# Kernel optimization log

Measured on AMD Instinct MI355X. Metric: run time of the kernel, lower is better.

## Reference

```python
import jax, jax.numpy as jnp
import numpy as np

H = 1024        # hidden_dim
MD = 2048       # memory_dim
L = 16384       # memory length == max_length
N = 8           # head_N
# sys.float_info.min underflows to 0.0 in float32, exactly as in the torch
# original (python float * float32 tensor). Kept for faithfulness.
TINY = jnp.float32(2.2250738585072014e-308)


def setup_inputs() -> dict:
    key = jax.random.key(0)
    ks = jax.random.split(key, 12)
    s_h = 1.0 / np.sqrt(H)
    s_m = 1.0 / np.sqrt(MD)
    s_o = 1.0 / np.sqrt(2 * H)
    return {
        "x": jax.random.normal(ks[0], (1, 1, H), jnp.float32),
        "memory": jax.random.normal(ks[1], (L, MD), jnp.float32),
        "Wq": jax.random.uniform(ks[2], (H, H), jnp.float32, -s_h, s_h),
        "bq": jax.random.uniform(ks[3], (H,), jnp.float32, -s_h, s_h),
        "Wk": jax.random.uniform(ks[4], (H, MD), jnp.float32, -s_m, s_m),
        "bk": jax.random.uniform(ks[5], (H,), jnp.float32, -s_m, s_m),
        "Wv": jax.random.uniform(ks[6], (H, MD), jnp.float32, -s_m, s_m),
        "bv": jax.random.uniform(ks[7], (H,), jnp.float32, -s_m, s_m),
        "Wo": jax.random.uniform(ks[8], (H, 2 * H), jnp.float32, -s_o, s_o),
        "bo": jax.random.uniform(ks[9], (H,), jnp.float32, -s_o, s_o),
    }


def reference(x, memory, Wq, bq, Wk, bk, Wv, bv, Wo, bo):
    d = H // N  # per-head dim
    # Q: (1,H) -> (1,d,N) -> (N,1,d), scaled by d**-0.5
    q = x.reshape(1, -1) @ Wq.T + bq
    Q = q.reshape(1, d, N).transpose(2, 0, 1) * (d ** -0.5)
    # K: (L,H) -> (L,d,N) -> (N,d,L)
    K = (memory @ Wk.T + bk).reshape(-1, d, N).transpose(2, 1, 0)
    QK = jnp.einsum('nod,ndl->nol', Q, K)  # (N,1,L)
    # pad mask: 1 where the memory row sums to zero, else 0 (as in torch nonzero-set)
    any_zero = memory.sum(axis=1)
    pad_mask = (any_zero == 0).astype(QK.dtype)[None, None, :]
    QK = QK + pad_mask * TINY
    attn = jax.nn.softmax(QK, axis=-1)
    # V: (L,H) -> (L,d,N) -> (N,L,d)
    V = (memory @ Wv.T + bv).reshape(-1, d, N).transpose(2, 0, 1)
    feat = jnp.einsum('nol,nld->nod', attn, V)      # (N,1,d)
    feat = feat.transpose(1, 2, 0).reshape(1, 1, H)  # (1,1,H)
    ax = jnp.concatenate([x, feat], axis=-1)         # (1,1,2H)
    return jax.nn.relu(ax @ Wo.T + bo)
```

## Files before the change

kernel.cpp:

```cpp
#include <hip/hip_runtime.h>
#include <math.h>

#define LROWS 16384
#define HDIM  1024
#define MDIM  2048
#define RSQRT_D 0.08838834764831844f

#define OFF_W     0
#define OFF_BETA  16384
#define OFF_Z     16392
#define OFF_Q     16400
#define OFF_FEAT  17424
#define OFF_Y     18448
#define OFF_ZP    34832
#define OFF_S2    38928
#define OFF_YBUF  301072

__device__ __forceinline__ float dot4(float4 a, float4 b) {
  return a.x * b.x + a.y * b.y + a.z * b.z + a.w * b.w;
}
__device__ __forceinline__ void fma4(float4& acc, float s, float4 v) {
  acc.x = fmaf(s, v.x, acc.x); acc.y = fmaf(s, v.y, acc.y);
  acc.z = fmaf(s, v.z, acc.z); acc.w = fmaf(s, v.w, acc.w);
}
__device__ __forceinline__ void add4(float4& a, float4 v) {
  a.x += v.x; a.y += v.y; a.z += v.z; a.w += v.w;
}

__global__ __launch_bounds__(256) void kq(const float* __restrict__ x,
                                          const float* __restrict__ Wq,
                                          const float* __restrict__ bq,
                                          float* __restrict__ ws) {
  int tid = threadIdx.x, lane = tid & 63;
  int j = blockIdx.x * 4 + (tid >> 6);
  const float4* xr = (const float4*)x;
  const float4* wr = (const float4*)(Wq + (size_t)j * HDIM);
  float acc = 0.f;
#pragma unroll
  for (int i = 0; i < 4; ++i) {
    int idx = i * 64 + lane;
    acc += dot4(xr[idx], wr[idx]);
  }
#pragma unroll
  for (int off = 32; off; off >>= 1) acc += __shfl_xor(acc, off);
  if (lane == 0) ws[OFF_Q + j] = acc + bq[j];
  if (tid < 64) ws[OFF_W + blockIdx.x * 64 + tid] = 0.f;
}

__global__ __launch_bounds__(256) void kw(const float* __restrict__ Wk,
                                          const float* __restrict__ bk,
                                          float* __restrict__ ws) {
  __shared__ float lds[32];
  int tid = threadIdx.x;
  const float* q = ws + OFF_Q;
  if (blockIdx.x == 256) {
    float b = 0.f;
#pragma unroll
    for (int i = 0; i < 4; ++i) {
      int c = tid + 256 * i;
      b = fmaf(q[c], bk[c], b);
    }
    b += __shfl_xor(b, 8); b += __shfl_xor(b, 16); b += __shfl_xor(b, 32);
    if ((tid & 63) < 8) lds[(tid >> 6) * 8 + (tid & 7)] = b;
    __syncthreads();
    if (tid < 8)
      ws[OFF_BETA + tid] = lds[tid] + lds[8 + tid] + lds[16 + tid] + lds[24 + tid];
    return;
  }
  int mc = blockIdx.x & 7, cc = blockIdx.x >> 3;
  int m = mc * 256 + tid;
  float acc[8];
#pragma unroll
  for (int n = 0; n < 8; ++n) acc[n] = 0.f;
  int c0 = cc * 32;
#pragma unroll
  for (int cb = 0; cb < 32; cb += 8) {
#pragma unroll
    for (int u = 0; u < 8; ++u)
      acc[u] = fmaf(q[c0 + cb + u], Wk[(size_t)(c0 + cb + u) * MDIM + m], acc[u]);
  }
#pragma unroll
  for (int n = 0; n < 8; ++n) atomicAdd(&ws[OFF_W + n * MDIM + m], acc[n]);
}

__global__ __launch_bounds__(256, 4) void kA3(const float* __restrict__ mem,
                                              float* __restrict__ ws) {
  __shared__ float4 wlds[2048];
  int tid = threadIdx.x, lane = tid & 63, wv = tid >> 6;
  int ch = blockIdx.x & 1, rg = blockIdx.x >> 1;
  const float4* wsrc = (const float4*)(ws + OFF_W + ch * 1024);
#pragma unroll
  for (int k = 0; k < 8; ++k) {
    int qi = k * 256 + tid;
    wlds[qi] = wsrc[(qi >> 8) * 512 + (qi & 255)];
  }
  __syncthreads();

  int r0 = rg * 32 + wv * 8;
  const float* base = mem + (size_t)r0 * MDIM + ch * 1024;
  float* sbase = ws + OFF_S2 + (size_t)ch * 131072 + (size_t)r0 * 8;

  float4 mv[4], mvn[4];
#pragma unroll
  for (int i = 0; i < 4; ++i)
    mv[i] = *(const float4*)(base + (i * 64 + lane) * 4);

#pragma unroll
  for (int rl = 0; rl < 8; ++rl) {
    if (rl < 7) {
#pragma unroll
      for (int i = 0; i < 4; ++i)
        mvn[i] = *(const float4*)(base + (size_t)(rl + 1) * MDIM + (i * 64 + lane) * 4);
    }
    float acc[8];
#pragma unroll
    for (int n = 0; n < 8; ++n) acc[n] = 0.f;
#pragma unroll
    for (int pass = 0; pass < 4; ++pass) {
      int cq = pass * 64 + lane;
#pragma unroll
      for (int n = 0; n < 8; ++n) {
        float4 w4 = wlds[n * 256 + cq];
        acc[n] = fmaf(mv[pass].x, w4.x, acc[n]);
        acc[n] = fmaf(mv[pass].y, w4.y, acc[n]);
        acc[n] = fmaf(mv[pass].z, w4.z, acc[n]);
        acc[n] = fmaf(mv[pass].w, w4.w, acc[n]);
      }
    }
#pragma unroll
    for (int off = 1; off < 64; off <<= 1)
#pragma unroll
      for (int n = 0; n < 8; ++n)
        acc[n] += __shfl_xor(acc[n], off);
    if (lane == 0) {
      float4* dst = (float4*)(sbase + rl * 8);
      dst[0] = make_float4(acc[0], acc[1], acc[2], acc[3]);
      dst[1] = make_float4(acc[4], acc[5], acc[6], acc[7]);
    }
#pragma unroll
    for (int i = 0; i < 4; ++i) mv[i] = mvn[i];
  }
}

__global__ __launch_bounds__(256, 4) void kb(const float* __restrict__ mem,
                                             float* __restrict__ ws) {
  __shared__ __align__(16) float pp[256];
  __shared__ float zz[32];
  int tid = threadIdx.x, lane = tid & 63, wv = tid >> 6;
  int rc = blockIdx.x >> 1, ch = blockIdx.x & 1;
  int r0 = rc * 32;
  {
    int n = tid & 7;
    int r = r0 + (tid >> 3);
    float s0 = ws[OFF_S2 + (size_t)r * 8 + n];
    float s1 = ws[OFF_S2 + 131072 + (size_t)r * 8 + n];
    float p = __expf((s0 + s1 + ws[OFF_BETA + n]) * RSQRT_D);
    pp[tid] = p;
    if (ch == 0) {
      float z = p;
      z += __shfl_xor(z, 8); z += __shfl_xor(z, 16); z += __shfl_xor(z, 32);
      if (lane < 8) zz[wv * 8 + lane] = z;
    }
  }
  __syncthreads();
  if (ch == 0 && tid < 8)
    ws[OFF_ZP + rc * 8 + tid] = zz[tid] + zz[8 + tid] + zz[16 + tid] + zz[24 + tid];

  float4 acc[8];
#pragma unroll
  for (int n = 0; n < 8; ++n) acc[n] = make_float4(0.f, 0.f, 0.f, 0.f);
  const float* base = mem + (size_t)r0 * MDIM + ch * 1024 + tid * 4;
  const float4* pp4 = (const float4*)pp;
#pragma unroll 4
  for (int r = 0; r < 32; ++r) {
    float4 mv = *(const float4*)(base + (size_t)r * MDIM);
    float4 pA = pp4[r * 2], pB = pp4[r * 2 + 1];
    fma4(acc[0], pA.x, mv); fma4(acc[1], pA.y, mv);
    fma4(acc[2], pA.z, mv); fma4(acc[3], pA.w, mv);
    fma4(acc[4], pB.x, mv); fma4(acc[5], pB.y, mv);
    fma4(acc[6], pB.z, mv); fma4(acc[7], pB.w, mv);
  }
  float* yb = ws + OFF_YBUF + (size_t)rc * 16384 + ch * 1024 + tid * 4;
#pragma unroll
  for (int n = 0; n < 8; ++n)
    *(float4*)(yb + n * MDIM) = acc[n];
}

__global__ __launch_bounds__(256) void ky(float* __restrict__ ws) {
  __shared__ __align__(16) float lds[96];
  int tid = threadIdx.x, lane = tid & 63, wv = tid >> 6;
  int bid = blockIdx.x;
  const float4* src = (const float4*)(ws + OFF_YBUF);
  int qd = bid * 4 + (tid & 3);
  int h = tid >> 2;
  float4 a = make_float4(0.f, 0.f, 0.f, 0.f);
#pragma unroll
  for (int i = 0; i < 8; ++i)
    add4(a, src[(size_t)(h + 64 * i) * 4096 + qd]);
#pragma unroll
  for (int off = 4; off < 64; off <<= 1) {
    a.x += __shfl_xor(a.x, off);
    a.y += __shfl_xor(a.y, off);
    a.z += __shfl_xor(a.z, off);
    a.w += __shfl_xor(a.w, off);
  }
  float4* sq = (float4*)lds;
  if (lane < 4) sq[wv * 4 + lane] = a;
  __syncthreads();
  if (tid < 4) {
    float4 s = sq[tid];
    add4(s, sq[4 + tid]); add4(s, sq[8 + tid]); add4(s, sq[12 + tid]);
    ((float4*)(ws + OFF_Y))[bid * 4 + tid] = s;
  }
  if (bid == 0) {
    int n = tid & 7;
    float z = 0.f;
#pragma unroll
    for (int i = 0; i < 16; ++i)
      z += ws[OFF_ZP + ((tid >> 3) + 32 * i) * 8 + n];
    z += __shfl_xor(z, 8); z += __shfl_xor(z, 16); z += __shfl_xor(z, 32);
    float* zzz = lds + 64;
    if (lane < 8) zzz[wv * 8 + lane] = z;
    __syncthreads();
    if (tid < 8)
      ws[OFF_Z + tid] = zzz[tid] + zzz[8 + tid] + zzz[16 + tid] + zzz[24 + tid];
  }
}

__global__ __launch_bounds__(256) void kf(const float* __restrict__ Wv,
                                          const float* __restrict__ bv,
                                          float* __restrict__ ws) {
  int tid = threadIdx.x, lane = tid & 63;
  int c = blockIdx.x * 4 + (tid >> 6);
  int n = c & 7;
  const float4* yb = (const float4*)(ws + OFF_Y + n * MDIM);
  const float4* wb = (const float4*)(Wv + (size_t)c * MDIM);
  float acc = 0.f;
#pragma unroll
  for (int s = 0; s < 8; ++s) {
    int idx = s * 64 + lane;
    acc += dot4(yb[idx], wb[idx]);
  }
#pragma unroll
  for (int off = 32; off; off >>= 1) acc += __shfl_xor(acc, off);
  if (lane == 0) ws[OFF_FEAT + c] = acc / ws[OFF_Z + n] + bv[c];
}

__global__ __launch_bounds__(256) void ko(const float* __restrict__ x,
                                          const float* __restrict__ Wo,
                                          const float* __restrict__ bo,
                                          const float* __restrict__ ws,
                                          float* __restrict__ out) {
  int tid = threadIdx.x, lane = tid & 63;
  int j = blockIdx.x * 4 + (tid >> 6);
  const float4* wb = (const float4*)(Wo + (size_t)j * 2048);
  const float4* xr = (const float4*)x;
  const float4* fr = (const float4*)(ws + OFF_FEAT);
  float acc = 0.f;
#pragma unroll
  for (int s = 0; s < 4; ++s) {
    int idx = s * 64 + lane;
    acc += dot4(xr[idx], wb[idx]);
    acc += dot4(fr[idx], wb[256 + idx]);
  }
#pragma unroll
  for (int off = 32; off; off >>= 1) acc += __shfl_xor(acc, off);
  if (lane == 0) out[j] = fmaxf(acc + bo[j], 0.f);
}

extern "C" void kernel_launch(void* const* d_in, const int* in_sizes, int n_in,
                              void* d_out, int out_size, void* d_ws, size_t ws_size,
                              hipStream_t stream) {
  const float* x   = (const float*)d_in[0];
  const float* mem = (const float*)d_in[1];
  const float* Wq  = (const float*)d_in[2];
  const float* bq  = (const float*)d_in[3];
  const float* Wk  = (const float*)d_in[4];
  const float* bk  = (const float*)d_in[5];
  const float* Wv  = (const float*)d_in[6];
  const float* bv  = (const float*)d_in[7];
  const float* Wo  = (const float*)d_in[8];
  const float* bo  = (const float*)d_in[9];
  float* ws  = (float*)d_ws;
  float* out = (float*)d_out;

  kq <<<256,  256, 0, stream>>>(x, Wq, bq, ws);
  kw <<<257,  256, 0, stream>>>(Wk, bk, ws);
  kA3<<<1024, 256, 0, stream>>>(mem, ws);
  kb <<<1024, 256, 0, stream>>>(mem, ws);
  ky <<<1024, 256, 0, stream>>>(ws);
  kf <<<256,  256, 0, stream>>>(Wv, bv, ws);
  ko <<<256,  256, 0, stream>>>(x, Wo, bo, ws, out);
}
```

Baseline: 273.9 us.

## Fuse score and weighted-sum passes over memory into one kernel

Merges the score kernel and the softmax-weighted memory accumulation kernel into a single 512-thread block per 32 rows. Scores are reduced, exponentiated and kept in LDS instead of written to a global scratch buffer, and the same rows are re-read immediately for the weighted sum, so they are likely cache-resident. This removes a launch and a global round trip for the scores, at the cost of larger LDS use (full Wk-projected vector) and possibly lower occupancy.

```diff
diff --git a/kernel.cpp b/kernel.cpp
--- a/kernel.cpp
+++ b/kernel.cpp
@@ -1,7 +1,6 @@
 #include <hip/hip_runtime.h>
 #include <math.h>
 
-#define LROWS 16384
 #define HDIM  1024
 #define MDIM  2048
 #define RSQRT_D 0.08838834764831844f
@@ -13,7 +12,6 @@
 #define OFF_FEAT  17424
 #define OFF_Y     18448
 #define OFF_ZP    34832
-#define OFF_S2    38928
 #define OFF_YBUF  301072
 
 __device__ __forceinline__ float dot4(float4 a, float4 b) {
@@ -83,35 +81,38 @@
   for (int n = 0; n < 8; ++n) atomicAdd(&ws[OFF_W + n * MDIM + m], acc[n]);
 }
 
-__global__ __launch_bounds__(256, 4) void kA3(const float* __restrict__ mem,
+__global__ __launch_bounds__(512, 4) void kab(const float* __restrict__ mem,
                                               float* __restrict__ ws) {
-  __shared__ float4 wlds[2048];
+  __shared__ float4 wlds[4096];
+  __shared__ __align__(16) float pp[256];
+  __shared__ float zz[64];
+  __shared__ float bb[8];
   int tid = threadIdx.x, lane = tid & 63, wv = tid >> 6;
-  int ch = blockIdx.x & 1, rg = blockIdx.x >> 1;
-  const float4* wsrc = (const float4*)(ws + OFF_W + ch * 1024);
-#pragma unroll
-  for (int k = 0; k < 8; ++k) {
-    int qi = k * 256 + tid;
-    wlds[qi] = wsrc[(qi >> 8) * 512 + (qi & 255)];
-  }
+  int bid = blockIdx.x;
+  int r0 = bid * 32;
+
+  const float4* wsrc = (const float4*)(ws + OFF_W);
+#pragma unroll
+  for (int k = 0; k < 8; ++k)
+    wlds[k * 512 + tid] = wsrc[k * 512 + tid];
+  if (tid < 8) bb[tid] = ws[OFF_BETA + tid];
+
+  const float* rowp = mem + (size_t)(r0 + wv * 4) * MDIM;
+  float4 mva[4], mvan[4], mvb[4];
+#pragma unroll
+  for (int i = 0; i < 4; ++i)
+    mva[i] = *(const float4*)(rowp + (i * 64 + lane) * 4);
   __syncthreads();
 
-  int r0 = rg * 32 + wv * 8;
-  const float* base = mem + (size_t)r0 * MDIM + ch * 1024;
-  float* sbase = ws + OFF_S2 + (size_t)ch * 131072 + (size_t)r0 * 8;
-
-  float4 mv[4], mvn[4];
-#pragma unroll
-  for (int i = 0; i < 4; ++i)
-    mv[i] = *(const float4*)(base + (i * 64 + lane) * 4);
-
-#pragma unroll
-  for (int rl = 0; rl < 8; ++rl) {
-    if (rl < 7) {
-#pragma unroll
-      for (int i = 0; i < 4; ++i)
-        mvn[i] = *(const float4*)(base + (size_t)(rl + 1) * MDIM + (i * 64 + lane) * 4);
-    }
+  float zacc[8];
+#pragma unroll
+  for (int n = 0; n < 8; ++n) zacc[n] = 0.f;
+
+#pragma unroll
+  for (int rl = 0; rl < 4; ++rl) {
+#pragma unroll
+    for (int i = 0; i < 4; ++i)
+      mvb[i] = *(const float4*)(rowp + 1024 + (i * 64 + lane) * 4);
     float acc[8];
 #pragma unroll
     for (int n = 0; n < 8; ++n) acc[n] = 0.f;
@@ -120,11 +121,28 @@
       int cq = pass * 64 + lane;
 #pragma unroll
       for (int n = 0; n < 8; ++n) {
-        float4 w4 = wlds[n * 256 + cq];
-        acc[n] = fmaf(mv[pass].x, w4.x, acc[n]);
-        acc[n] = fmaf(mv[pass].y, w4.y, acc[n]);
-        acc[n] = fmaf(mv[pass].z, w4.z, acc[n]);
-        acc[n] = fmaf(mv[pass].w, w4.w, acc[n]);
+        float4 w4 = wlds[n * 512 + cq];
+        acc[n] = fmaf(mva[pass].x, w4.x, acc[n]);
+        acc[n] = fmaf(mva[pass].y, w4.y, acc[n]);
+        acc[n] = fmaf(mva[pass].z, w4.z, acc[n]);
+        acc[n] = fmaf(mva[pass].w, w4.w, acc[n]);
+      }
+    }
+    if (rl < 3) {
+#pragma unroll
+      for (int i = 0; i < 4; ++i)
+        mvan[i] = *(const float4*)(rowp + MDIM + (i * 64 + lane) * 4);
+    }
+#pragma unroll
+    for (int pass = 0; pass < 4; ++pass) {
+      int cq = 256 + pass * 64 + lane;
+#pragma unroll
+      for (int n = 0; n < 8; ++n) {
+        float4 w4 = wlds[n * 512 + cq];
+        acc[n] = fmaf(mvb[pass].x, w4.x, acc[n]);
+        acc[n] = fmaf(mvb[pass].y, w4.y, acc[n]);
+        acc[n] = fmaf(mvb[pass].z, w4.z, acc[n]);
+        acc[n] = fmaf(mvb[pass].w, w4.w, acc[n]);
       }
     }
 #pragma unroll
@@ -132,58 +150,46 @@
 #pragma unroll
       for (int n = 0; n < 8; ++n)
         acc[n] += __shfl_xor(acc[n], off);
-    if (lane == 0) {
-      float4* dst = (float4*)(sbase + rl * 8);
-      dst[0] = make_float4(acc[0], acc[1], acc[2], acc[3]);
-      dst[1] = make_float4(acc[4], acc[5], acc[6], acc[7]);
-    }
-#pragma unroll
-    for (int i = 0; i < 4; ++i) mv[i] = mvn[i];
-  }
-}
-
-__global__ __launch_bounds__(256, 4) void kb(const float* __restrict__ mem,
-                                             float* __restrict__ ws) {
-  __shared__ __align__(16) float pp[256];
-  __shared__ float zz[32];
-  int tid = threadIdx.x, lane = tid & 63, wv = tid >> 6;
-  int rc = blockIdx.x >> 1, ch = blockIdx.x & 1;
-  int r0 = rc * 32;
-  {
-    int n = tid & 7;
-    int r = r0 + (tid >> 3);
-    float s0 = ws[OFF_S2 + (size_t)r * 8 + n];
-    float s1 = ws[OFF_S2 + 131072 + (size_t)r * 8 + n];
-    float p = __expf((s0 + s1 + ws[OFF_BETA + n]) * RSQRT_D);
-    pp[tid] = p;
-    if (ch == 0) {
-      float z = p;
-      z += __shfl_xor(z, 8); z += __shfl_xor(z, 16); z += __shfl_xor(z, 32);
-      if (lane < 8) zz[wv * 8 + lane] = z;
-    }
+#pragma unroll
+    for (int n = 0; n < 8; ++n) {
+      float p = __expf((acc[n] + bb[n]) * RSQRT_D);
+      zacc[n] += p;
+      if (lane == 0) pp[(wv * 4 + rl) * 8 + n] = p;
+    }
+#pragma unroll
+    for (int i = 0; i < 4; ++i) mva[i] = mvan[i];
+    rowp += MDIM;
+  }
+  if (lane == 0) {
+#pragma unroll
+    for (int n = 0; n < 8; ++n) zz[wv * 8 + n] = zacc[n];
   }
   __syncthreads();
-  if (ch == 0 && tid < 8)
-    ws[OFF_ZP + rc * 8 + tid] = zz[tid] + zz[8 + tid] + zz[16 + tid] + zz[24 + tid];
-
-  float4 acc[8];
-#pragma unroll
-  for (int n = 0; n < 8; ++n) acc[n] = make_float4(0.f, 0.f, 0.f, 0.f);
-  const float* base = mem + (size_t)r0 * MDIM + ch * 1024 + tid * 4;
+  if (tid < 8) {
+    float z = 0.f;
+#pragma unroll
+    for (int w = 0; w < 8; ++w) z += zz[w * 8 + tid];
+    ws[OFF_ZP + bid * 8 + tid] = z;
+  }
+
+  float4 acc4[8];
+#pragma unroll
+  for (int n = 0; n < 8; ++n) acc4[n] = make_float4(0.f, 0.f, 0.f, 0.f);
+  const float* base = mem + (size_t)r0 * MDIM + tid * 4;
   const float4* pp4 = (const float4*)pp;
 #pragma unroll 4
   for (int r = 0; r < 32; ++r) {
     float4 mv = *(const float4*)(base + (size_t)r * MDIM);
     float4 pA = pp4[r * 2], pB = pp4[r * 2 + 1];
-    fma4(acc[0], pA.x, mv); fma4(acc[1], pA.y, mv);
-    fma4(acc[2], pA.z, mv); fma4(acc[3], pA.w, mv);
-    fma4(acc[4], pB.x, mv); fma4(acc[5], pB.y, mv);
-    fma4(acc[6], pB.z, mv); fma4(acc[7], pB.w, mv);
-  }
-  float* yb = ws + OFF_YBUF + (size_t)rc * 16384 + ch * 1024 + tid * 4;
+    fma4(acc4[0], pA.x, mv); fma4(acc4[1], pA.y, mv);
+    fma4(acc4[2], pA.z, mv); fma4(acc4[3], pA.w, mv);
+    fma4(acc4[4], pB.x, mv); fma4(acc4[5], pB.y, mv);
+    fma4(acc4[6], pB.z, mv); fma4(acc4[7], pB.w, mv);
+  }
+  float* yb = ws + OFF_YBUF + (size_t)bid * 16384 + tid * 4;
 #pragma unroll
   for (int n = 0; n < 8; ++n)
-    *(float4*)(yb + n * MDIM) = acc[n];
+    *(float4*)(yb + n * MDIM) = acc4[n];
 }
 
 __global__ __launch_bounds__(256) void ky(float* __restrict__ ws) {
@@ -284,11 +290,10 @@
   float* ws  = (float*)d_ws;
   float* out = (float*)d_out;
 
-  kq <<<256,  256, 0, stream>>>(x, Wq, bq, ws);
-  kw <<<257,  256, 0, stream>>>(Wk, bk, ws);
-  kA3<<<1024, 256, 0, stream>>>(mem, ws);
-  kb <<<1024, 256, 0, stream>>>(mem, ws);
+  kq <<<256, 256, 0, stream>>>(x, Wq, bq, ws);
+  kw <<<257, 256, 0, stream>>>(Wk, bk, ws);
+  kab<<<512, 512, 0, stream>>>(mem, ws);
   ky <<<1024, 256, 0, stream>>>(ws);
-  kf <<<256,  256, 0, stream>>>(Wv, bv, ws);
-  ko <<<256,  256, 0, stream>>>(x, Wo, bo, ws, out);
-}
+  kf <<<256, 256, 0, stream>>>(Wv, bv, ws);
+  ko <<<256, 256, 0, stream>>>(x, Wo, bo, ws, out);
+}
```

Measured after the change: 262.9 us. 4.0% less time.
